# Optimization experiments

Measured on AMD Instinct MI355X. Metric: run time of the kernel, lower is better.

The kernel has to match this reference:

```python
import jax, jax.numpy as jnp
import numpy as np

N = 100000   # num nodes
E = 1600000  # num edges
D = 64       # feature / hidden dim (irreps_in == hidden_dim)
SCALE = D ** -0.5


def setup_inputs() -> dict:
    key = jax.random.key(0)
    ks = jax.random.split(key, 6)
    x = jax.random.normal(ks[0], (N, D), dtype=jnp.float32)
    edge_index = jax.random.randint(ks[1], (2, E), 0, N, dtype=jnp.int32)
    std = D ** -0.5
    Wq = jax.random.normal(ks[2], (D, D), dtype=jnp.float32) * std
    Wk = jax.random.normal(ks[3], (D, D), dtype=jnp.float32) * std
    Wv = jax.random.normal(ks[4], (D, D), dtype=jnp.float32) * std
    Wo = jax.random.normal(ks[5], (D, D), dtype=jnp.float32) * std
    return {"x": x, "edge_index": edge_index, "Wq": Wq, "Wk": Wk, "Wv": Wv, "Wo": Wo}


def reference(x, edge_index, Wq, Wk, Wv, Wo):
    # Per-receiver variable-length attention over incoming neighbors.
    # Mathematically identical to the torch module's degree-bucketed SDPA
    # (softmax over each node's neighbor set), without padding buffers.
    sender, receiver = edge_index[0], edge_index[1]
    Q = x @ Wq  # [N, D]
    K = x @ Wk
    V = x @ Wv
    # per-edge logits: <Q[receiver], K[sender]> * scale
    s = jnp.einsum('ed,ed->e', Q[receiver], K[sender]) * SCALE  # [E]
    # numerically stable segment softmax over receiver groups
    m = jax.ops.segment_max(s, receiver, num_segments=N)  # -inf for empty segments
    m_safe = jnp.where(jnp.isfinite(m), m, 0.0)
    p = jnp.exp(s - m_safe[receiver])  # [E]
    denom = jax.ops.segment_sum(p, receiver, num_segments=N)  # [N]
    num = jax.ops.segment_sum(p[:, None] * V[sender], receiver, num_segments=N)  # [N, D]
    # zero-degree nodes get out = 0 (matches torch: skipped buckets + nan_to_num)
    out = jnp.where(denom[:, None] > 0,
                    num / jnp.maximum(denom, 1e-30)[:, None],
                    0.0)
    return x + out @ Wo
```

## Files before the change

kernel.cpp:

```cpp
#include <hip/hip_runtime.h>
#include <hip/hip_bf16.h>

#define DIM 64
#define SCALE 0.125f
#define BINSH 5
#define NPB 32
#define BCAP 768
#define CHUNK 16384
#define MAXBINS 3200

static __device__ __forceinline__ unsigned int pack2bf(float a, float b) {
    unsigned int ua = __float_as_uint(a), ub = __float_as_uint(b);
    ua += 0x7fffu + ((ua >> 16) & 1u);
    ub += 0x7fffu + ((ub >> 16) & 1u);
    return (ua >> 16) | (ub & 0xffff0000u);
}
static __device__ __forceinline__ float2 unpack2bf(unsigned int u) {
    return make_float2(__uint_as_float(u << 16), __uint_as_float(u & 0xffff0000u));
}

__global__ __launch_bounds__(256) void k_wmul(const float* __restrict__ Wv,
                                              const float* __restrict__ Wo,
                                              float* __restrict__ Wvo) {
    __shared__ __align__(16) float av[64 * 64];
    __shared__ __align__(16) float bo[64 * 64];
    int tid = threadIdx.x;
    for (int i = tid; i < 1024; i += 256) {
        ((float4*)av)[i] = ((const float4*)Wv)[i];
        ((float4*)bo)[i] = ((const float4*)Wo)[i];
    }
    __syncthreads();
    int r = tid >> 2, c0 = (tid & 3) * 16;
    float acc[16];
#pragma unroll
    for (int j = 0; j < 16; j++) acc[j] = 0.f;
    for (int k = 0; k < 64; k++) {
        float a = av[r * 64 + k];
#pragma unroll
        for (int j = 0; j < 16; j++)
            acc[j] = fmaf(a, bo[k * 64 + c0 + j], acc[j]);
    }
#pragma unroll
    for (int j = 0; j < 16; j++) Wvo[r * 64 + c0 + j] = acc[j];
}

__global__ __launch_bounds__(1024) void k_binA(const int* __restrict__ send,
                                               const int* __restrict__ recv,
                                               int* __restrict__ binCur,
                                               unsigned int* __restrict__ ebufA,
                                               int E, int NBK) {
    __shared__ int hist[MAXBINS];
    __shared__ int lcur[MAXBINS];
    int tid = threadIdx.x;
    int base = blockIdx.x * CHUNK;
    int lim = min(base + CHUNK, E);

    for (int i = tid; i < NBK; i += 1024) hist[i] = 0;
    __syncthreads();
    for (int i = base + tid; i < lim; i += 1024)
        atomicAdd(&hist[recv[i] >> BINSH], 1);
    __syncthreads();
    for (int i = tid; i < NBK; i += 1024) {
        int h = hist[i];
        lcur[i] = h ? atomicAdd(&binCur[i], h) : 0;
    }
    __syncthreads();
    for (int i = base + tid; i < lim; i += 1024) {
        int r = recv[i];
        int b = r >> BINSH;
        int p = atomicAdd(&lcur[b], 1);
        if (p < BCAP)
            ebufA[(size_t)b * BCAP + p] = (unsigned)send[i] | ((unsigned)(r & (NPB - 1)) << 17);
    }
}

__global__ __launch_bounds__(256) void k_qkv(const float* __restrict__ x,
                                             const float* __restrict__ Wq,
                                             const float* __restrict__ Wk,
                                             const float* __restrict__ Wvo,
                                             float* __restrict__ Q,
                                             unsigned int* __restrict__ KVb,
                                             int N, int nchunk) {
    __shared__ __align__(16) float ws[64 * 64];
    __shared__ __align__(16) float xs[4][64 * 64];
    int tid = threadIdx.x;
    int wv = tid >> 6;
    int lane = tid & 63;
    int m = blockIdx.x / nchunk;
    int cb = blockIdx.x % nchunk;
    const float* W = (m == 0) ? Wq : ((m == 1) ? Wk : Wvo);

    for (int i = tid; i < 1024; i += 256) ((float4*)ws)[i] = ((const float4*)W)[i];
    __syncthreads();

    int base = cb * 256 + wv * 64;
    if (base < N) {
        float* xw = xs[wv];
#pragma unroll
        for (int c4 = 0; c4 < 16; c4++) {
            float4 v = make_float4(0.f, 0.f, 0.f, 0.f);
            if (base + lane < N) v = ((const float4*)x)[(size_t)(base + lane) * 16 + c4];
            xw[(c4 * 4 + 0) * 64 + lane] = v.x;
            xw[(c4 * 4 + 1) * 64 + lane] = v.y;
            xw[(c4 * 4 + 2) * 64 + lane] = v.z;
            xw[(c4 * 4 + 3) * 64 + lane] = v.w;
        }
        asm volatile("s_waitcnt lgkmcnt(0)" ::: "memory");

        int lr = lane >> 3;
        int lc = lane & 7;
        const float* xp = xw + lr * 8;
        const float* wp = ws + lc * 8;

        float acc[8][8];
#pragma unroll
        for (int i = 0; i < 8; i++)
#pragma unroll
            for (int j = 0; j < 8; j++) acc[i][j] = 0.f;

        float4 xa = *(const float4*)(xp);
        float4 xb = *(const float4*)(xp + 4);
        float4 wa = *(const float4*)(wp);
        float4 wb = *(const float4*)(wp + 4);
#pragma unroll 4
        for (int k = 0; k < 64; k++) {
            float4 xan, xbn, wan, wbn;
            if (k < 63) {
                xan = *(const float4*)(xp + (k + 1) * 64);
                xbn = *(const float4*)(xp + (k + 1) * 64 + 4);
                wan = *(const float4*)(wp + (k + 1) * 64);
                wbn = *(const float4*)(wp + (k + 1) * 64 + 4);
            }
            float xv[8] = {xa.x, xa.y, xa.z, xa.w, xb.x, xb.y, xb.z, xb.w};
            float wc[8] = {wa.x, wa.y, wa.z, wa.w, wb.x, wb.y, wb.z, wb.w};
#pragma unroll
            for (int i = 0; i < 8; i++)
#pragma unroll
                for (int j = 0; j < 8; j++)
                    acc[i][j] = fmaf(xv[i], wc[j], acc[i][j]);
            xa = xan; xb = xbn; wa = wan; wb = wbn;
        }

#pragma unroll
        for (int i = 0; i < 8; i++) {
            int row = base + lr * 8 + i;
            if (row < N) {
                if (m == 0) {
                    float* dst = &Q[(size_t)row * 64 + lc * 8];
                    ((float4*)dst)[0] = make_float4(acc[i][0], acc[i][1], acc[i][2], acc[i][3]);
                    ((float4*)dst)[1] = make_float4(acc[i][4], acc[i][5], acc[i][6], acc[i][7]);
                } else {
                    unsigned int* dst = &KVb[(size_t)row * 64 + (m - 1) * 32 + lc * 4];
                    uint4 pk;
                    pk.x = pack2bf(acc[i][0], acc[i][1]);
                    pk.y = pack2bf(acc[i][2], acc[i][3]);
                    pk.z = pack2bf(acc[i][4], acc[i][5]);
                    pk.w = pack2bf(acc[i][6], acc[i][7]);
                    *((uint4*)dst) = pk;
                }
            }
        }
    }
}

__global__ __launch_bounds__(256) void k_attn(const float* __restrict__ Q,
                                              const unsigned int* __restrict__ KVb,
                                              const float* __restrict__ x,
                                              const int* __restrict__ binCur,
                                              const unsigned int* __restrict__ ebufA,
                                              float* __restrict__ out, int N) {
    __shared__ unsigned int llist[BCAP];
    __shared__ int ldeg[NPB], lofs[NPB + 1], lcur[NPB];
    int tid = threadIdx.x;
    int wv = tid >> 6;
    int lane = tid & 63;
    int g = lane >> 3;
    int sub = lane & 7;

    int j = blockIdx.x;
    int cnt = min(binCur[j], BCAP);
    const unsigned int* ebin = ebufA + (size_t)j * BCAP;

    if (tid < NPB) ldeg[tid] = 0;
    __syncthreads();

    for (int i = tid; i < cnt; i += 256)
        atomicAdd(&ldeg[(ebin[i] >> 17) & (NPB - 1)], 1);
    __syncthreads();

    if (wv == 0 && lane < NPB) {
        int d = ldeg[lane];
        int s = d;
        for (int o = 1; o < NPB; o <<= 1) {
            int t = __shfl_up(s, o, NPB);
            if ((lane & (NPB - 1)) >= o) s += t;
        }
        lofs[lane + 1] = s;
        lcur[lane] = s - d;
        if (lane == 0) lofs[0] = 0;
    }
    __syncthreads();

    for (int i = tid; i < cnt; i += 256) {
        unsigned int u = ebin[i];
        int n = (u >> 17) & (NPB - 1);
        int p = atomicAdd(&lcur[n], 1);
        llist[p] = u & 0x1FFFFu;
    }
    __syncthreads();

    for (int n = wv; n < NPB; n += 4) {
        int r = (j << BINSH) + n;
        if (r >= N) break;
        int start = lofs[n];
        int end = lofs[n + 1];
        float4 qa = *((const float4*)&Q[(size_t)r * 64 + sub * 8]);
        float4 qb = *((const float4*)&Q[(size_t)r * 64 + sub * 8 + 4]);
        float q[8] = {qa.x, qa.y, qa.z, qa.w, qb.x, qb.y, qb.z, qb.w};
        float acc[8] = {0.f, 0.f, 0.f, 0.f, 0.f, 0.f, 0.f, 0.f};
        float dpart = 0.f;

        int eA = start + g;
        bool vA = eA < end;
        unsigned int sA = vA ? llist[eA] : 0u;
        uint4 kA = *((const uint4*)&KVb[(size_t)sA * 64 + sub * 4]);
        uint4 uA = *((const uint4*)&KVb[(size_t)sA * 64 + 32 + sub * 4]);
        int eB = start + 8 + g;
        bool vB = eB < end;
        unsigned int sB = vB ? llist[eB] : 0u;
        uint4 kB = *((const uint4*)&KVb[(size_t)sB * 64 + sub * 4]);
        uint4 uB = *((const uint4*)&KVb[(size_t)sB * 64 + 32 + sub * 4]);

        for (int bb = start; bb < end; bb += 8) {
            int eC = bb + 16 + g;
            bool vC = eC < end;
            unsigned int sC = vC ? llist[eC] : 0u;
            uint4 kC = *((const uint4*)&KVb[(size_t)sC * 64 + sub * 4]);
            uint4 uC = *((const uint4*)&KVb[(size_t)sC * 64 + 32 + sub * 4]);

            float2 k01 = unpack2bf(kA.x), k23 = unpack2bf(kA.y);
            float2 k45 = unpack2bf(kA.z), k67 = unpack2bf(kA.w);
            float dot = q[0] * k01.x + q[1] * k01.y + q[2] * k23.x + q[3] * k23.y
                      + q[4] * k45.x + q[5] * k45.y + q[6] * k67.x + q[7] * k67.y;
            dot += __shfl_xor(dot, 1);
            dot += __shfl_xor(dot, 2);
            dot += __shfl_xor(dot, 4);
            float w = vA ? __expf(dot * SCALE) : 0.f;

            float2 v01 = unpack2bf(uA.x), v23 = unpack2bf(uA.y);
            float2 v45 = unpack2bf(uA.z), v67 = unpack2bf(uA.w);
            acc[0] = fmaf(w, v01.x, acc[0]);
            acc[1] = fmaf(w, v01.y, acc[1]);
            acc[2] = fmaf(w, v23.x, acc[2]);
            acc[3] = fmaf(w, v23.y, acc[3]);
            acc[4] = fmaf(w, v45.x, acc[4]);
            acc[5] = fmaf(w, v45.y, acc[5]);
            acc[6] = fmaf(w, v67.x, acc[6]);
            acc[7] = fmaf(w, v67.y, acc[7]);
            dpart += w;

            kA = kB; uA = uB; vA = vB;
            kB = kC; uB = uC; vB = vC;
        }

        dpart += __shfl_xor(dpart, 8); dpart += __shfl_xor(dpart, 16); dpart += __shfl_xor(dpart, 32);
#pragma unroll
        for (int jj = 0; jj < 8; jj++) {
            acc[jj] += __shfl_xor(acc[jj], 8);
            acc[jj] += __shfl_xor(acc[jj], 16);
            acc[jj] += __shfl_xor(acc[jj], 32);
        }

        float inv = (dpart > 0.f) ? (1.0f / dpart) : 0.f;

        if (g == 0) {
            float4 xa = *((const float4*)&x[(size_t)r * 64 + sub * 8]);
            float4 xb = *((const float4*)&x[(size_t)r * 64 + sub * 8 + 4]);
            float4 oa = make_float4(fmaf(acc[0], inv, xa.x), fmaf(acc[1], inv, xa.y),
                                    fmaf(acc[2], inv, xa.z), fmaf(acc[3], inv, xa.w));
            float4 ob = make_float4(fmaf(acc[4], inv, xb.x), fmaf(acc[5], inv, xb.y),
                                    fmaf(acc[6], inv, xb.z), fmaf(acc[7], inv, xb.w));
            *((float4*)&out[(size_t)r * 64 + sub * 8]) = oa;
            *((float4*)&out[(size_t)r * 64 + sub * 8 + 4]) = ob;
        }
    }
}


extern "C" void kernel_launch(void* const* d_in, const int* in_sizes, int n_in,
                              void* d_out, int out_size, void* d_ws, size_t ws_size,
                              hipStream_t stream) {
    const float* x  = (const float*)d_in[0];
    const int* edge = (const int*)d_in[1];
    const float* Wq = (const float*)d_in[2];
    const float* Wk = (const float*)d_in[3];
    const float* Wv = (const float*)d_in[4];
    const float* Wo = (const float*)d_in[5];
    float* out = (float*)d_out;

    int N = in_sizes[0] / DIM;
    int E = in_sizes[1] / 2;
    int NBK = (N + NPB - 1) >> BINSH;

    char* p = (char*)d_ws;
    auto cv = [&](size_t bytes) {
        char* r = p;
        p += ((bytes + 255) / 256) * 256;
        return r;
    };
    float*        Q      = (float*)cv((size_t)N * 64 * 4);
    unsigned int* KVb    = (unsigned int*)cv((size_t)N * 64 * 4);
    float*        Wvo    = (float*)cv(64 * 64 * 4);
    int*          binCur = (int*)cv((size_t)NBK * 4);
    unsigned int* ebufA  = (unsigned int*)cv((size_t)NBK * BCAP * 4);
    (void)ws_size; (void)n_in; (void)out_size;

    const int* send = edge;
    const int* recv = edge + E;

    hipMemsetAsync(binCur, 0, (size_t)NBK * 4, stream);
    k_binA<<<(E + CHUNK - 1) / CHUNK, 1024, 0, stream>>>(send, recv, binCur, ebufA, E, NBK);
    k_wmul<<<1, 256, 0, stream>>>(Wv, Wo, Wvo);
    int nchunk = (N + 255) / 256;
    k_qkv<<<3 * nchunk, 256, 0, stream>>>(x, Wq, Wk, Wvo, Q, KVb, N, nchunk);
    k_attn<<<NBK, 256, 0, stream>>>(Q, KVb, x, binCur, ebufA, out, N);
}
```

Measured before the change: 236.4 us.

## Split bin counters into sub-buckets, fuse weight multiply into binning, deepen prefetch

Each bin's global counter and edge buffer is split into 8 sub-buckets chosen by block index. This reduces contention on the global atomics when many chunk blocks append to the same bin. The Wv·Wo product moves into block 0 of the binning kernel, which removes one launch. The attention loop's gather prefetch grows from two to three edge groups ahead to hide more latency. The cost is a segmented read in the attention kernel, more register pressure, and a per-sub-bucket capacity of 192 that could drop edges if the edges are skewed.

Result: no change. 239.4 us (+1.3%).

```diff
diff --git a/kernel.cpp b/kernel.cpp
--- a/kernel.cpp
+++ b/kernel.cpp
@@ -5,7 +5,9 @@
 #define SCALE 0.125f
 #define BINSH 5
 #define NPB 32
-#define BCAP 768
+#define NBKT 8
+#define SCAP 192
+#define LLCAP (NBKT * SCAP)
 #define CHUNK 16384
 #define MAXBINS 3200
 
@@ -19,39 +21,38 @@
     return make_float2(__uint_as_float(u << 16), __uint_as_float(u & 0xffff0000u));
 }
 
-__global__ __launch_bounds__(256) void k_wmul(const float* __restrict__ Wv,
-                                              const float* __restrict__ Wo,
-                                              float* __restrict__ Wvo) {
-    __shared__ __align__(16) float av[64 * 64];
-    __shared__ __align__(16) float bo[64 * 64];
+__global__ __launch_bounds__(1024) void k_prep(const int* __restrict__ send,
+                                               const int* __restrict__ recv,
+                                               const float* __restrict__ Wv,
+                                               const float* __restrict__ Wo,
+                                               float* __restrict__ Wvo,
+                                               int* __restrict__ binCur,
+                                               unsigned int* __restrict__ ebuf,
+                                               int E, int NBK) {
+    __shared__ __align__(16) float smem[8192];
+    int* hist = (int*)smem;
+    int* lcur = hist + MAXBINS;
     int tid = threadIdx.x;
-    for (int i = tid; i < 1024; i += 256) {
-        ((float4*)av)[i] = ((const float4*)Wv)[i];
-        ((float4*)bo)[i] = ((const float4*)Wo)[i];
-    }
-    __syncthreads();
-    int r = tid >> 2, c0 = (tid & 3) * 16;
-    float acc[16];
-#pragma unroll
-    for (int j = 0; j < 16; j++) acc[j] = 0.f;
-    for (int k = 0; k < 64; k++) {
-        float a = av[r * 64 + k];
-#pragma unroll
-        for (int j = 0; j < 16; j++)
-            acc[j] = fmaf(a, bo[k * 64 + c0 + j], acc[j]);
-    }
-#pragma unroll
-    for (int j = 0; j < 16; j++) Wvo[r * 64 + c0 + j] = acc[j];
-}
-
-__global__ __launch_bounds__(1024) void k_binA(const int* __restrict__ send,
-                                               const int* __restrict__ recv,
-                                               int* __restrict__ binCur,
-                                               unsigned int* __restrict__ ebufA,
-                                               int E, int NBK) {
-    __shared__ int hist[MAXBINS];
-    __shared__ int lcur[MAXBINS];
-    int tid = threadIdx.x;
+
+    if (blockIdx.x == 0) {
+        float* av = smem;
+        float* bo = smem + 4096;
+        ((float4*)av)[tid] = ((const float4*)Wv)[tid];
+        ((float4*)bo)[tid] = ((const float4*)Wo)[tid];
+        __syncthreads();
+        int r = tid >> 4, c0 = (tid & 15) * 4;
+        float acc[4] = {0.f, 0.f, 0.f, 0.f};
+        for (int k = 0; k < 64; k++) {
+            float a = av[r * 64 + k];
+#pragma unroll
+            for (int j = 0; j < 4; j++) acc[j] = fmaf(a, bo[k * 64 + c0 + j], acc[j]);
+        }
+#pragma unroll
+        for (int j = 0; j < 4; j++) Wvo[r * 64 + c0 + j] = acc[j];
+        __syncthreads();
+    }
+
+    int bucket = blockIdx.x & (NBKT - 1);
     int base = blockIdx.x * CHUNK;
     int lim = min(base + CHUNK, E);
 
@@ -62,15 +63,16 @@
     __syncthreads();
     for (int i = tid; i < NBK; i += 1024) {
         int h = hist[i];
-        lcur[i] = h ? atomicAdd(&binCur[i], h) : 0;
+        lcur[i] = h ? atomicAdd(&binCur[i * NBKT + bucket], h) : 0;
     }
     __syncthreads();
     for (int i = base + tid; i < lim; i += 1024) {
         int r = recv[i];
         int b = r >> BINSH;
         int p = atomicAdd(&lcur[b], 1);
-        if (p < BCAP)
-            ebufA[(size_t)b * BCAP + p] = (unsigned)send[i] | ((unsigned)(r & (NPB - 1)) << 17);
+        if (p < SCAP)
+            ebuf[((size_t)b * NBKT + bucket) * SCAP + p] =
+                (unsigned)send[i] | ((unsigned)(r & (NPB - 1)) << 17);
     }
 }
 
@@ -167,10 +169,11 @@
                                               const unsigned int* __restrict__ KVb,
                                               const float* __restrict__ x,
                                               const int* __restrict__ binCur,
-                                              const unsigned int* __restrict__ ebufA,
+                                              const unsigned int* __restrict__ ebuf,
                                               float* __restrict__ out, int N) {
-    __shared__ unsigned int llist[BCAP];
+    __shared__ unsigned int llist[LLCAP];
     __shared__ int ldeg[NPB], lofs[NPB + 1], lcur[NPB];
+    __shared__ int segc[NBKT];
     int tid = threadIdx.x;
     int wv = tid >> 6;
     int lane = tid & 63;
@@ -178,14 +181,17 @@
     int sub = lane & 7;
 
     int j = blockIdx.x;
-    int cnt = min(binCur[j], BCAP);
-    const unsigned int* ebin = ebufA + (size_t)j * BCAP;
-
+    const unsigned int* ebin = ebuf + (size_t)j * NBKT * SCAP;
+
+    if (tid < NBKT) segc[tid] = min(binCur[j * NBKT + tid], SCAP);
     if (tid < NPB) ldeg[tid] = 0;
     __syncthreads();
 
-    for (int i = tid; i < cnt; i += 256)
-        atomicAdd(&ldeg[(ebin[i] >> 17) & (NPB - 1)], 1);
+    for (int s = 0; s < NBKT; s++) {
+        int c = segc[s];
+        for (int i = tid; i < c; i += 256)
+            atomicAdd(&ldeg[(ebin[s * SCAP + i] >> 17) & (NPB - 1)], 1);
+    }
     __syncthreads();
 
     if (wv == 0 && lane < NPB) {
@@ -201,11 +207,14 @@
     }
     __syncthreads();
 
-    for (int i = tid; i < cnt; i += 256) {
-        unsigned int u = ebin[i];
-        int n = (u >> 17) & (NPB - 1);
-        int p = atomicAdd(&lcur[n], 1);
-        llist[p] = u & 0x1FFFFu;
+    for (int s = 0; s < NBKT; s++) {
+        int c = segc[s];
+        for (int i = tid; i < c; i += 256) {
+            unsigned int u = ebin[s * SCAP + i];
+            int n = (u >> 17) & (NPB - 1);
+            int p = atomicAdd(&lcur[n], 1);
+            llist[p] = u & 0x1FFFFu;
+        }
     }
     __syncthreads();
 
@@ -230,13 +239,18 @@
         unsigned int sB = vB ? llist[eB] : 0u;
         uint4 kB = *((const uint4*)&KVb[(size_t)sB * 64 + sub * 4]);
         uint4 uB = *((const uint4*)&KVb[(size_t)sB * 64 + 32 + sub * 4]);
+        int eC = start + 16 + g;
+        bool vC = eC < end;
+        unsigned int sC = vC ? llist[eC] : 0u;
+        uint4 kC = *((const uint4*)&KVb[(size_t)sC * 64 + sub * 4]);
+        uint4 uC = *((const uint4*)&KVb[(size_t)sC * 64 + 32 + sub * 4]);
 
         for (int bb = start; bb < end; bb += 8) {
-            int eC = bb + 16 + g;
-            bool vC = eC < end;
-            unsigned int sC = vC ? llist[eC] : 0u;
-            uint4 kC = *((const uint4*)&KVb[(size_t)sC * 64 + sub * 4]);
-            uint4 uC = *((const uint4*)&KVb[(size_t)sC * 64 + 32 + sub * 4]);
+            int eD = bb + 24 + g;
+            bool vD = eD < end;
+            unsigned int sD = vD ? llist[eD] : 0u;
+            uint4 kD = *((const uint4*)&KVb[(size_t)sD * 64 + sub * 4]);
+            uint4 uD = *((const uint4*)&KVb[(size_t)sD * 64 + 32 + sub * 4]);
 
             float2 k01 = unpack2bf(kA.x), k23 = unpack2bf(kA.y);
             float2 k45 = unpack2bf(kA.z), k67 = unpack2bf(kA.w);
@@ -261,6 +275,7 @@
 
             kA = kB; uA = uB; vA = vB;
             kB = kC; uB = uC; vB = vC;
+            kC = kD; uC = uD; vC = vD;
         }
 
         dpart += __shfl_xor(dpart, 8); dpart += __shfl_xor(dpart, 16); dpart += __shfl_xor(dpart, 32);
@@ -311,17 +326,17 @@
     float*        Q      = (float*)cv((size_t)N * 64 * 4);
     unsigned int* KVb    = (unsigned int*)cv((size_t)N * 64 * 4);
     float*        Wvo    = (float*)cv(64 * 64 * 4);
-    int*          binCur = (int*)cv((size_t)NBK * 4);
-    unsigned int* ebufA  = (unsigned int*)cv((size_t)NBK * BCAP * 4);
+    int*          binCur = (int*)cv((size_t)NBK * NBKT * 4);
+    unsigned int* ebuf   = (unsigned int*)cv((size_t)NBK * NBKT * SCAP * 4);
     (void)ws_size; (void)n_in; (void)out_size;
 
     const int* send = edge;
     const int* recv = edge + E;
 
-    hipMemsetAsync(binCur, 0, (size_t)NBK * 4, stream);
-    k_binA<<<(E + CHUNK - 1) / CHUNK, 1024, 0, stream>>>(send, recv, binCur, ebufA, E, NBK);
-    k_wmul<<<1, 256, 0, stream>>>(Wv, Wo, Wvo);
+    hipMemsetAsync(binCur, 0, (size_t)NBK * NBKT * 4, stream);
+    k_prep<<<(E + CHUNK - 1) / CHUNK, 1024, 0, stream>>>(send, recv, Wv, Wo, Wvo,
+                                                         binCur, ebuf, E, NBK);
     int nchunk = (N + 255) / 256;
     k_qkv<<<3 * nchunk, 256, 0, stream>>>(x, Wq, Wk, Wvo, Q, KVb, N, nchunk);
-    k_attn<<<NBK, 256, 0, stream>>>(Q, KVb, x, binCur, ebufA, out, N);
-}
+    k_attn<<<NBK, 256, 0, stream>>>(Q, KVb, x, binCur, ebuf, out, N);
+}
```

## Fuse edge binning, Wv·Wo product, and QKV projection into one launch

Applied to the files above, without the earlier changes.

Merges the edge-binning kernel, the single-block Wv·Wo multiply and the QKV projection kernel into one launch. The first blocks do binning and the rest do projections, and each V-block recomputes Wvo locally in shared memory. This removes two kernel launches and the serial dependency on the tiny Wvo kernel, so binning and projection can overlap. In exchange, binning blocks shrink from 1024 to 256 threads, every V-block redoes a 64x64 matmul, and shared memory grows to 80KB per block, which may reduce occupancy.

After: 241.7 us. 2.3% more time.

```diff
diff --git a/kernel.cpp b/kernel.cpp
--- a/kernel.cpp
+++ b/kernel.cpp
@@ -19,83 +19,88 @@
     return make_float2(__uint_as_float(u << 16), __uint_as_float(u & 0xffff0000u));
 }
 
-__global__ __launch_bounds__(256) void k_wmul(const float* __restrict__ Wv,
-                                              const float* __restrict__ Wo,
-                                              float* __restrict__ Wvo) {
-    __shared__ __align__(16) float av[64 * 64];
-    __shared__ __align__(16) float bo[64 * 64];
-    int tid = threadIdx.x;
-    for (int i = tid; i < 1024; i += 256) {
-        ((float4*)av)[i] = ((const float4*)Wv)[i];
-        ((float4*)bo)[i] = ((const float4*)Wo)[i];
-    }
-    __syncthreads();
-    int r = tid >> 2, c0 = (tid & 3) * 16;
-    float acc[16];
-#pragma unroll
-    for (int j = 0; j < 16; j++) acc[j] = 0.f;
-    for (int k = 0; k < 64; k++) {
-        float a = av[r * 64 + k];
-#pragma unroll
-        for (int j = 0; j < 16; j++)
-            acc[j] = fmaf(a, bo[k * 64 + c0 + j], acc[j]);
-    }
-#pragma unroll
-    for (int j = 0; j < 16; j++) Wvo[r * 64 + c0 + j] = acc[j];
-}
-
-__global__ __launch_bounds__(1024) void k_binA(const int* __restrict__ send,
+__global__ __launch_bounds__(256) void k_fused(const int* __restrict__ send,
                                                const int* __restrict__ recv,
+                                               const float* __restrict__ x,
+                                               const float* __restrict__ Wq,
+                                               const float* __restrict__ Wk,
+                                               const float* __restrict__ Wv,
+                                               const float* __restrict__ Wo,
                                                int* __restrict__ binCur,
                                                unsigned int* __restrict__ ebufA,
-                                               int E, int NBK) {
-    __shared__ int hist[MAXBINS];
-    __shared__ int lcur[MAXBINS];
+                                               float* __restrict__ Q,
+                                               unsigned int* __restrict__ KVb,
+                                               int E, int N, int NBK,
+                                               int NBIN, int nchunk) {
+    __shared__ __align__(16) float smem[20480];
     int tid = threadIdx.x;
-    int base = blockIdx.x * CHUNK;
-    int lim = min(base + CHUNK, E);
-
-    for (int i = tid; i < NBK; i += 1024) hist[i] = 0;
-    __syncthreads();
-    for (int i = base + tid; i < lim; i += 1024)
-        atomicAdd(&hist[recv[i] >> BINSH], 1);
-    __syncthreads();
-    for (int i = tid; i < NBK; i += 1024) {
-        int h = hist[i];
-        lcur[i] = h ? atomicAdd(&binCur[i], h) : 0;
-    }
-    __syncthreads();
-    for (int i = base + tid; i < lim; i += 1024) {
-        int r = recv[i];
-        int b = r >> BINSH;
-        int p = atomicAdd(&lcur[b], 1);
-        if (p < BCAP)
-            ebufA[(size_t)b * BCAP + p] = (unsigned)send[i] | ((unsigned)(r & (NPB - 1)) << 17);
-    }
-}
-
-__global__ __launch_bounds__(256) void k_qkv(const float* __restrict__ x,
-                                             const float* __restrict__ Wq,
-                                             const float* __restrict__ Wk,
-                                             const float* __restrict__ Wvo,
-                                             float* __restrict__ Q,
-                                             unsigned int* __restrict__ KVb,
-                                             int N, int nchunk) {
-    __shared__ __align__(16) float ws[64 * 64];
-    __shared__ __align__(16) float xs[4][64 * 64];
-    int tid = threadIdx.x;
+
+    if ((int)blockIdx.x < NBIN) {
+        int* hist = (int*)smem;
+        int* lcur = hist + MAXBINS;
+        int base = blockIdx.x * CHUNK;
+        int lim = min(base + CHUNK, E);
+
+        for (int i = tid; i < NBK; i += 256) hist[i] = 0;
+        __syncthreads();
+        for (int i = base + tid; i < lim; i += 256)
+            atomicAdd(&hist[recv[i] >> BINSH], 1);
+        __syncthreads();
+        for (int i = tid; i < NBK; i += 256) {
+            int h = hist[i];
+            lcur[i] = h ? atomicAdd(&binCur[i], h) : 0;
+        }
+        __syncthreads();
+        for (int i = base + tid; i < lim; i += 256) {
+            int r = recv[i];
+            int b = r >> BINSH;
+            int p = atomicAdd(&lcur[b], 1);
+            if (p < BCAP)
+                ebufA[(size_t)b * BCAP + p] =
+                    (unsigned)send[i] | ((unsigned)(r & (NPB - 1)) << 17);
+        }
+        return;
+    }
+
+    float* ws = smem;
+    float* xs = smem + 4096;
     int wv = tid >> 6;
     int lane = tid & 63;
-    int m = blockIdx.x / nchunk;
-    int cb = blockIdx.x % nchunk;
-    const float* W = (m == 0) ? Wq : ((m == 1) ? Wk : Wvo);
-
-    for (int i = tid; i < 1024; i += 256) ((float4*)ws)[i] = ((const float4*)W)[i];
-    __syncthreads();
+    int qb = blockIdx.x - NBIN;
+    int m = qb / nchunk;
+    int cb = qb % nchunk;
+
+    if (m < 2) {
+        const float* W = (m == 0) ? Wq : Wk;
+        for (int i = tid; i < 1024; i += 256) ((float4*)ws)[i] = ((const float4*)W)[i];
+        __syncthreads();
+    } else {
+        float* av = xs;
+        float* bo = xs + 4096;
+        for (int i = tid; i < 1024; i += 256) {
+            ((float4*)av)[i] = ((const float4*)Wv)[i];
+            ((float4*)bo)[i] = ((const float4*)Wo)[i];
+        }
+        __syncthreads();
+        int r = tid >> 2, c0 = (tid & 3) * 16;
+        float wvo[16];
+#pragma unroll
+        for (int j = 0; j < 16; j++) wvo[j] = 0.f;
+        for (int k = 0; k < 64; k++) {
+            float a = av[r * 64 + k];
+#pragma unroll
+            for (int j = 0; j < 16; j++)
+                wvo[j] = fmaf(a, bo[k * 64 + c0 + j], wvo[j]);
+        }
+        __syncthreads();
+#pragma unroll
+        for (int j = 0; j < 16; j++) ws[r * 64 + c0 + j] = wvo[j];
+        __syncthreads();
+    }
 
     int base = cb * 256 + wv * 64;
     if (base < N) {
-        float* xw = xs[wv];
+        float* xw = xs + wv * 4096;
 #pragma unroll
         for (int c4 = 0; c4 < 16; c4++) {
             float4 v = make_float4(0.f, 0.f, 0.f, 0.f);
@@ -310,7 +315,6 @@
     };
     float*        Q      = (float*)cv((size_t)N * 64 * 4);
     unsigned int* KVb    = (unsigned int*)cv((size_t)N * 64 * 4);
-    float*        Wvo    = (float*)cv(64 * 64 * 4);
     int*          binCur = (int*)cv((size_t)NBK * 4);
     unsigned int* ebufA  = (unsigned int*)cv((size_t)NBK * BCAP * 4);
     (void)ws_size; (void)n_in; (void)out_size;
@@ -318,10 +322,12 @@
     const int* send = edge;
     const int* recv = edge + E;
 
+    int NBIN = (E + CHUNK - 1) / CHUNK;
+    int nchunk = (N + 255) / 256;
+
     hipMemsetAsync(binCur, 0, (size_t)NBK * 4, stream);
-    k_binA<<<(E + CHUNK - 1) / CHUNK, 1024, 0, stream>>>(send, recv, binCur, ebufA, E, NBK);
-    k_wmul<<<1, 256, 0, stream>>>(Wv, Wo, Wvo);
-    int nchunk = (N + 255) / 256;
-    k_qkv<<<3 * nchunk, 256, 0, stream>>>(x, Wq, Wk, Wvo, Q, KVb, N, nchunk);
+    k_fused<<<NBIN + 3 * nchunk, 256, 0, stream>>>(send, recv, x, Wq, Wk, Wv, Wo,
+                                                   binCur, ebufA, Q, KVb,
+                                                   E, N, NBK, NBIN, nchunk);
     k_attn<<<NBK, 256, 0, stream>>>(Q, KVb, x, binCur, ebufA, out, N);
 }
```
